# Kernel optimization log

Measured on AMD Instinct MI355X. Metric: run time of the kernel, lower is better.

Reference implementation:

```python
import jax, jax.numpy as jnp
import numpy as np

NJ, NS = 30000, 12000            # num job / skill nodes
E_JS, E_SJ, E_SS = 300000, 300000, 150000
SBERT, HID, OUT = 384, 128, 128
H = 2                             # GAT heads (concat=True)
NEG_SLOPE = 0.2


def setup_inputs() -> dict:
    key = jax.random.key(0)
    ks = iter(jax.random.split(key, 64))
    nrm = lambda shape, s=1.0: jax.random.normal(next(ks), shape, jnp.float32) * s
    ridx = lambda n, hi: jax.random.randint(next(ks), (n,), 0, hi, jnp.int32)
    W = 0.05  # weight scale to keep activations sane across layers
    return dict(
        x_job=nrm((NJ, SBERT)), x_skill=nrm((NS, SBERT)),
        ei_js_src=ridx(E_JS, NJ), ei_js_dst=ridx(E_JS, NS),
        ei_sj_src=ridx(E_SJ, NS), ei_sj_dst=ridx(E_SJ, NJ),
        ei_ss_src=ridx(E_SS, NS), ei_ss_dst=ridx(E_SS, NS),
        query=nrm((SBERT,)),
        W0_job=nrm((SBERT, HID), W), b0_job=jnp.zeros((HID,), jnp.float32),
        g0_job=jnp.ones((HID,), jnp.float32), be0_job=jnp.zeros((HID,), jnp.float32),
        W0_skill=nrm((SBERT, HID), W), b0_skill=jnp.zeros((HID,), jnp.float32),
        g0_skill=jnp.ones((HID,), jnp.float32), be0_skill=jnp.zeros((HID,), jnp.float32),
        gat_Ws=nrm((2, 3, HID, H * HID), W), gat_Wd=nrm((2, 3, HID, H * HID), W),
        gat_as=nrm((2, 3, H, HID), W), gat_ad=nrm((2, 3, H, HID), W),
        gat_b=jnp.zeros((2, 3, H * HID), jnp.float32),
        inter_W=nrm((2, 2, H * HID, HID), W), inter_b=jnp.zeros((2, 2, HID), jnp.float32),
        Wjf=nrm((HID, OUT), W), bjf=jnp.zeros((OUT,), jnp.float32),
        Wq=nrm((SBERT, OUT), W), bq=jnp.zeros((OUT,), jnp.float32),
    )


def _layer_norm(x, g, b):
    mu = x.mean(-1, keepdims=True)
    var = ((x - mu) ** 2).mean(-1, keepdims=True)
    return (x - mu) * jax.lax.rsqrt(var + 1e-5) * g + b


def _gat(x_src, x_dst, src, dst, Ws, Wd, a_s, a_d, bias, num_dst):
    # PyG GATConv: lin_src/lin_dst (no bias), additive attention, scatter-softmax over dst.
    hs = (x_src @ Ws).reshape(-1, H, HID)            # [Ns,H,C]
    hd = (x_dst @ Wd).reshape(-1, H, HID)            # [Nd,H,C]
    e = jax.nn.leaky_relu((hs * a_s).sum(-1)[src] + (hd * a_d).sum(-1)[dst], NEG_SLOPE)  # [E,H]
    m = jax.ops.segment_max(e, dst, num_segments=num_dst)
    p = jnp.exp(e - m[dst])
    den = jax.ops.segment_sum(p, dst, num_segments=num_dst)
    w = p / (den[dst] + 1e-16)                       # [E,H]
    out = jax.ops.segment_sum(hs[src] * w[:, :, None], dst, num_segments=num_dst)
    return out.reshape(num_dst, H * HID) + bias


def _forward(x_job, x_skill, query,
             W0_job, b0_job, g0_job, be0_job, W0_skill, b0_skill, g0_skill, be0_skill,
             gat_Ws, gat_Wd, gat_as, gat_ad, gat_b, inter_W, inter_b, Wjf, bjf, Wq, bq,
             ei_js_src, ei_js_dst, ei_sj_src, ei_sj_dst, ei_ss_src, ei_ss_dst):
    # initial per-type lin + LN + relu (dropout = identity in eval)
    xj = jax.nn.relu(_layer_norm(x_job @ W0_job + b0_job, g0_job, be0_job))
    xs = jax.nn.relu(_layer_norm(x_skill @ W0_skill + b0_skill, g0_skill, be0_skill))
    # skill->skill relation adds self loops (src == dst node type)
    loops = jnp.arange(NS, dtype=jnp.int32)
    ss_src = jnp.concatenate([ei_ss_src, loops])
    ss_dst = jnp.concatenate([ei_ss_dst, loops])
    for i in range(2):  # num_layers
        o_s = (_gat(xj, xs, ei_js_src, ei_js_dst, gat_Ws[i, 0], gat_Wd[i, 0],
                    gat_as[i, 0], gat_ad[i, 0], gat_b[i, 0], NS)
               + _gat(xs, xs, ss_src, ss_dst, gat_Ws[i, 2], gat_Wd[i, 2],
                      gat_as[i, 2], gat_ad[i, 2], gat_b[i, 2], NS))  # HeteroConv aggr='sum'
        o_j = _gat(xs, xj, ei_sj_src, ei_sj_dst, gat_Ws[i, 1], gat_Wd[i, 1],
                   gat_as[i, 1], gat_ad[i, 1], gat_b[i, 1], NJ)
        xj = jax.nn.relu(o_j @ inter_W[i, 0] + inter_b[i, 0])
        xs = jax.nn.relu(o_s @ inter_W[i, 1] + inter_b[i, 1])
    job_emb = xj @ Wjf + bjf                          # [NJ,OUT]
    q = query @ Wq + bq                               # [OUT]
    scores = job_emb @ q                              # [NJ]
    return scores, job_emb, q


def reference(x_job, x_skill, ei_js_src, ei_js_dst, ei_sj_src, ei_sj_dst,
              ei_ss_src, ei_ss_dst, query,
              W0_job, b0_job, g0_job, be0_job, W0_skill, b0_skill, g0_skill, be0_skill,
              gat_Ws, gat_Wd, gat_as, gat_ad, gat_b, inter_W, inter_b,
              Wjf, bjf, Wq, bq):
    return _forward(x_job, x_skill, query,
                    W0_job, b0_job, g0_job, be0_job, W0_skill, b0_skill, g0_skill, be0_skill,
                    gat_Ws, gat_Wd, gat_as, gat_ad, gat_b, inter_W, inter_b, Wjf, bjf, Wq, bq,
                    ei_js_src, ei_js_dst, ei_sj_src, ei_sj_dst, ei_ss_src, ei_ss_dst)
```

## Files before the change

kernel.cpp:

```cpp
#include <hip/hip_runtime.h>
#include <hip/hip_bf16.h>
#include <math.h>

#define NJ 30000
#define NS 12000
#define E_JS 300000
#define E_SJ 300000
#define E_SS 150000
#define ETOT (E_JS + E_SJ + E_SS + NS)
#define NBINS (NS + NJ + NS)
#define NBUK ((NBINS + 63) / 64)
#define SBERT 384
#define HIST_NB 512
#define SCAT_NB 480
#define CAST_MATS 14
#define CAST_BPM 48
#define PREP_CAST (CAST_MATS * CAST_BPM)
#define PREP_WA   (PREP_CAST + 192)
#define PREP_QV   PREP_WA
#define PREP_GB   (PREP_QV + 1)
#define PREP_HIST (PREP_GB + 1)

static inline int cdiv(int a, int b) { return (a + b - 1) / b; }

typedef __attribute__((ext_vector_type(8))) short bf8_t;
typedef __attribute__((ext_vector_type(4))) float f4_t;
typedef unsigned short u16;

__device__ inline float bf2f(unsigned short u) {
    union { unsigned int i; float f; } z; z.i = ((unsigned int)u) << 16; return z.f;
}
__device__ inline unsigned short f2bf(float f) {
    unsigned int x = __float_as_uint(f);
    unsigned int r = (x + 0x7fffu + ((x >> 16) & 1u)) >> 16;
    return (unsigned short)r;
}

__device__ inline void edge_decode(int e, const int* js_src, const int* js_dst,
                                   const int* sj_src, const int* sj_dst,
                                   const int* ss_src, const int* ss_dst,
                                   int& src, int& bin) {
    if (e < E_JS) { src = js_src[e]; bin = js_dst[e]; }
    else if (e < E_JS + E_SJ) { int i = e - E_JS; src = sj_src[i]; bin = NS + sj_dst[i]; }
    else if (e < E_JS + E_SJ + E_SS) { int i = e - E_JS - E_SJ; src = ss_src[i]; bin = NS + NJ + ss_dst[i]; }
    else { int i = e - E_JS - E_SJ - E_SS; src = i; bin = NS + NJ + i; }
}

struct CastT { const float* src; unsigned short* dst; int K; int N; int srcLd; int dstLd; };
struct PrepArgs {
    CastT m[CAST_MATS];
    const float* Ws; const float* as_; const float* Wd; const float* ad_;
    float* wsa; float* wda; int* bcnt;
    const float* query; const float* Wq; const float* bq; float* qv;
    const float* gat_b; float* gbS;
    const int* js_src; const int* js_dst;
    const int* sj_src; const int* sj_dst;
    const int* ss_src; const int* ss_dst;
};

__global__ __launch_bounds__(256) void k_prep(PrepArgs A) {
    __shared__ float ldt[32][33];
    __shared__ int lh[NBUK];
    int b = blockIdx.x;
    if (b < PREP_CAST) {
        int mi = b / CAST_BPM, bx = b % CAST_BPM;
        CastT cm = A.m[mi];
        int tilesN = cm.N >> 5;
        int total = (cm.K >> 5) * tilesN;
        if (bx >= total) return;
        int tk = bx / tilesN, tn = bx % tilesN;
        int k0 = tk * 32, n0 = tn * 32;
        int col = threadIdx.x & 31;
        int row0 = threadIdx.x >> 5;
#pragma unroll
        for (int r = 0; r < 4; ++r) {
            int kk = row0 + r * 8;
            ldt[kk][col] = cm.src[(size_t)(k0 + kk) * cm.srcLd + n0 + col];
        }
        __syncthreads();
#pragma unroll
        for (int r = 0; r < 4; ++r) {
            int nn = row0 + r * 8;
            cm.dst[(size_t)(n0 + nn) * cm.dstLd + k0 + col] = f2bf(ldt[col][nn]);
        }
    } else if (b < PREP_WA) {
        int qw = ((b - PREP_CAST) * 256 + threadIdx.x) >> 4;
        int cl = threadIdx.x & 15;
        if (qw < 2 * 1536) {
            int which = qw / 1536;
            int r = qw % 1536;
            int lr = r / 256;
            int kh = r % 256;
            int k = kh / 2, h = kh % 2;
            const float* W = which ? A.Wd : A.Ws;
            const float* a = which ? A.ad_ : A.as_;
            const float* wrow = W + ((size_t)(lr * 128 + k)) * 256 + h * 128 + cl * 8;
            const float* arow = a + (size_t)(lr * 2 + h) * 128 + cl * 8;
            float4 w0 = *(const float4*)wrow, w1 = *(const float4*)(wrow + 4);
            float4 a0 = *(const float4*)arow, a1 = *(const float4*)(arow + 4);
            float acc = w0.x * a0.x + w0.y * a0.y + w0.z * a0.z + w0.w * a0.w
                      + w1.x * a1.x + w1.y * a1.y + w1.z * a1.z + w1.w * a1.w;
            acc += __shfl_xor(acc, 1, 64);
            acc += __shfl_xor(acc, 2, 64);
            acc += __shfl_xor(acc, 4, 64);
            acc += __shfl_xor(acc, 8, 64);
            if (cl == 0) (which ? A.wda : A.wsa)[lr * 256 + k * 2 + h] = acc;
        }
    } else if (b == PREP_QV) {
        int c = threadIdx.x;
        if (c < 128) {
            float acc = A.bq[c];
            for (int k = 0; k < SBERT; ++k) acc += A.query[k] * A.Wq[(size_t)k * 128 + c];
            A.qv[c] = acc;
        }
    } else if (b == PREP_GB) {
        int c = threadIdx.x;
        if (c < 256) A.gbS[c] = A.gat_b[c] + A.gat_b[512 + c];
    } else {
        int t = threadIdx.x;
        for (int i = t; i < NBUK; i += 256) lh[i] = 0;
        __syncthreads();
        int hb = b - PREP_HIST;
        for (int e = hb * 256 + t; e < ETOT; e += HIST_NB * 256) {
            int src, bin;
            edge_decode(e, A.js_src, A.js_dst, A.sj_src, A.sj_dst, A.ss_src, A.ss_dst, src, bin);
            atomicAdd(&lh[bin >> 6], 1);
        }
        __syncthreads();
        for (int i = t; i < NBUK; i += 256) {
            int v = lh[i];
            if (v) atomicAdd(&A.bcnt[i], v);
        }
    }
}

struct GJob {
    const void* X; const unsigned short* Wt;
    const float* bias; const float* gamma; const float* beta;
    void* Y; int M; int K; int N; int ldY; int srcf32;
    const float* qv; float* sc;
    int aMode = 0;
    const float* wav0 = nullptr; const float* wav1 = nullptr;
    const float* wav2 = nullptr; const float* wav3 = nullptr;
    float* aOut = nullptr; int aStride = 0;
};
struct GPair { GJob a; GJob b; int blocksA; };

template <int EPI>
__device__ void mgemm_body(const GPair& P, int bx) {
    int mb = bx;
    GJob g = (mb < P.blocksA) ? P.a : P.b;
    if (mb >= P.blocksA) mb -= P.blocksA;
    const int row0 = mb * 64;

    __shared__ __align__(16) float As[4][64][32];
    __shared__ __align__(16) unsigned short Bs[4][128][32];
    const int t = threadIdx.x;
    const int wave = t >> 6, lane = t & 63;
    const int q = lane >> 4, c = lane & 15;
    const int K = g.K;
    const float* Xf = (const float*)g.X;

    f4_t acc[8];
#pragma unroll
    for (int nt = 0; nt < 8; ++nt) acc[nt] = (f4_t){0.f, 0.f, 0.f, 0.f};

    auto STAGE = [&](int cur, int k0) {
#pragma unroll
        for (int i = 0; i < 2; ++i) {
            int bi = i * 256 + t;
            int row = bi >> 3, b = bi & 7;
            int ra = row0 + row; ra = (ra < g.M) ? ra : (g.M - 1);
            const float* gsrc = Xf + (size_t)ra * K + k0 + ((b ^ (row & 7)) << 2);
            __builtin_amdgcn_global_load_lds(
                (__attribute__((address_space(1))) void*)gsrc,
                (__attribute__((address_space(3))) void*)((char*)&As[cur][0][0] + ((i * 4 + wave) << 10)),
                16, 0, 0);
        }
#pragma unroll
        for (int i = 0; i < 2; ++i) {
            int bi = i * 256 + t;
            int row = bi >> 2, b = bi & 3;
            const unsigned short* gsrc = g.Wt + (size_t)row * K + k0 + ((b ^ ((row >> 1) & 3)) << 3);
            __builtin_amdgcn_global_load_lds(
                (__attribute__((address_space(1))) void*)gsrc,
                (__attribute__((address_space(3))) void*)((char*)&Bs[cur][0][0] + ((i * 4 + wave) << 10)),
                16, 0, 0);
        }
    };

    auto MF = [&](int cur) {
        const char* Ab = (const char*)&As[cur][0][0];
        const char* Bb = (const char*)&Bs[cur][0][0];
        int r = wave * 16 + c;
        int sw = r & 7;
        f4_t fa0 = *(const f4_t*)(Ab + r * 128 + (((q * 2) ^ sw) << 4));
        f4_t fa1 = *(const f4_t*)(Ab + r * 128 + (((q * 2 + 1) ^ sw) << 4));
        bf8_t af;
        af[0] = (short)f2bf(fa0[0]); af[1] = (short)f2bf(fa0[1]);
        af[2] = (short)f2bf(fa0[2]); af[3] = (short)f2bf(fa0[3]);
        af[4] = (short)f2bf(fa1[0]); af[5] = (short)f2bf(fa1[1]);
        af[6] = (short)f2bf(fa1[2]); af[7] = (short)f2bf(fa1[3]);
#pragma unroll
        for (int nt = 0; nt < 8; ++nt) {
            int rb = nt * 16 + c;
            bf8_t bfr = *(const bf8_t*)(Bb + rb * 64 + ((q ^ ((rb >> 1) & 3)) << 4));
            acc[nt] = __builtin_amdgcn_mfma_f32_16x16x32_bf16(af, bfr, acc[nt], 0, 0, 0);
        }
    };

    STAGE(0, 0);
    STAGE(1, 32);
    STAGE(2, 64);
#pragma unroll
    for (int k = 0; k < 12; ++k) {
        if (k < 10)      asm volatile("s_waitcnt vmcnt(8)" ::: "memory");
        else if (k == 10) asm volatile("s_waitcnt vmcnt(4)" ::: "memory");
        else             asm volatile("s_waitcnt vmcnt(0)" ::: "memory");
        __builtin_amdgcn_s_barrier();
        asm volatile("" ::: "memory");
        if (k + 3 < 12) STAGE((k + 3) & 3, (k + 3) * 32);
        MF(k & 3);
    }

    float bcol[8], gcol[8], becol[8];
#pragma unroll
    for (int nt = 0; nt < 8; ++nt) {
        bcol[nt] = g.bias[nt * 16 + c];
        if constexpr (EPI == 3) {
            gcol[nt] = g.gamma[nt * 16 + c];
            becol[nt] = g.beta[nt * 16 + c];
        }
    }

#pragma unroll
    for (int r = 0; r < 4; ++r) {
        int grow = row0 + wave * 16 + q * 4 + r;
        float v[8];
#pragma unroll
        for (int nt = 0; nt < 8; ++nt) v[nt] = acc[nt][r] + bcol[nt];
        if constexpr (EPI == 3) {
            float s = 0.f, ss = 0.f;
#pragma unroll
            for (int nt = 0; nt < 8; ++nt) { s += v[nt]; ss += v[nt] * v[nt]; }
#pragma unroll
            for (int m = 8; m >= 1; m >>= 1) {
                s += __shfl_xor(s, m, 64);
                ss += __shfl_xor(ss, m, 64);
            }
            float mu = s * (1.f / 128.f);
            float var = ss * (1.f / 128.f) - mu * mu;
            float rs = rsqrtf(var + 1e-5f);
#pragma unroll
            for (int nt = 0; nt < 8; ++nt)
                v[nt] = fmaxf((v[nt] - mu) * rs * gcol[nt] + becol[nt], 0.f);
        }
        if (g.aMode > 0) {
            float pa[8];
#pragma unroll
            for (int i = 0; i < 8; ++i) pa[i] = 0.f;
#pragma unroll
            for (int nt = 0; nt < 8; ++nt) {
                int col = nt * 16 + c;
                float2 w0 = *(const float2*)&g.wav0[col * 2];
                pa[0] += v[nt] * w0.x; pa[1] += v[nt] * w0.y;
                if (g.aMode > 1) {
                    float2 w1 = *(const float2*)&g.wav1[col * 2];
                    pa[2] += v[nt] * w1.x; pa[3] += v[nt] * w1.y;
                }
                if (g.aMode > 2) {
                    float2 w2 = *(const float2*)&g.wav2[col * 2];
                    float2 w3 = *(const float2*)&g.wav3[col * 2];
                    pa[4] += v[nt] * w2.x; pa[5] += v[nt] * w2.y;
                    pa[6] += v[nt] * w3.x; pa[7] += v[nt] * w3.y;
                }
            }
#pragma unroll
            for (int m = 8; m >= 1; m >>= 1) {
                pa[0] += __shfl_xor(pa[0], m, 64); pa[1] += __shfl_xor(pa[1], m, 64);
                pa[2] += __shfl_xor(pa[2], m, 64); pa[3] += __shfl_xor(pa[3], m, 64);
                pa[4] += __shfl_xor(pa[4], m, 64); pa[5] += __shfl_xor(pa[5], m, 64);
                pa[6] += __shfl_xor(pa[6], m, 64); pa[7] += __shfl_xor(pa[7], m, 64);
            }
            if (c == 0 && grow < g.M) {
                float* ao = &g.aOut[(size_t)grow * g.aStride];
                ao[0] = pa[0]; ao[1] = pa[1];
                if (g.aMode > 1) { ao[2] = pa[2]; ao[3] = pa[3]; }
                if (g.aMode > 2) { ao[4] = pa[4]; ao[5] = pa[5]; ao[6] = pa[6]; ao[7] = pa[7]; }
            }
        }
        if (grow < g.M) {
            unsigned short* Y = (unsigned short*)g.Y;
#pragma unroll
            for (int nt = 0; nt < 8; ++nt)
                Y[(size_t)grow * g.ldY + nt * 16 + c] = f2bf(v[nt]);
        }
    }
}

__global__ __launch_bounds__(256) void k_scan(
    const int* __restrict__ bcnt, int* __restrict__ bukoff, int* __restrict__ bukcur) {
    __shared__ int sd[256];
    int t = threadIdx.x;
    int i0 = t * 4;
    int v0 = (i0 < NBUK) ? bcnt[i0] : 0;
    int v1 = (i0 + 1 < NBUK) ? bcnt[i0 + 1] : 0;
    int v2 = (i0 + 2 < NBUK) ? bcnt[i0 + 2] : 0;
    int v3 = (i0 + 3 < NBUK) ? bcnt[i0 + 3] : 0;
    int csum = v0 + v1 + v2 + v3;
    sd[t] = csum;
    __syncthreads();
    for (int off = 1; off < 256; off <<= 1) {
        int tmp = (t >= off) ? sd[t - off] : 0;
        __syncthreads();
        sd[t] += tmp;
        __syncthreads();
    }
    int excl = sd[t] - csum;
    int p0 = excl, p1 = excl + v0, p2 = excl + v0 + v1, p3 = excl + v0 + v1 + v2;
    if (i0 < NBUK) { bukoff[i0] = p0; bukcur[i0] = p0; }
    if (i0 + 1 < NBUK) { bukoff[i0 + 1] = p1; bukcur[i0 + 1] = p1; }
    if (i0 + 2 < NBUK) { bukoff[i0 + 2] = p2; bukcur[i0 + 2] = p2; }
    if (i0 + 3 < NBUK) { bukoff[i0 + 3] = p3; bukcur[i0 + 3] = p3; }
    if (t == 0) bukoff[NBUK] = ETOT;
}

__global__ __launch_bounds__(256) void k_lin0_scat(
    GPair P, int gemmBlocks,
    const int* __restrict__ js_src, const int* __restrict__ js_dst,
    const int* __restrict__ sj_src, const int* __restrict__ sj_dst,
    const int* __restrict__ ss_src, const int* __restrict__ ss_dst,
    int* __restrict__ bukcur, uint2* __restrict__ pairs) {
    if (blockIdx.x < (unsigned)gemmBlocks) {
        mgemm_body<3>(P, blockIdx.x);
        return;
    }
    __shared__ int lh[NBUK];
    __shared__ int lbase[NBUK];
    int t = threadIdx.x;
    int sb = blockIdx.x - gemmBlocks;
    const int CH = (ETOT + SCAT_NB - 1) / SCAT_NB;
    const int beg = sb * CH;
    const int endi = (beg + CH < ETOT) ? beg + CH : ETOT;
    if (beg >= ETOT) return;
    for (int i = t; i < NBUK; i += 256) lh[i] = 0;
    __syncthreads();
    for (int e = beg + t; e < endi; e += 256) {
        int src, bin;
        edge_decode(e, js_src, js_dst, sj_src, sj_dst, ss_src, ss_dst, src, bin);
        atomicAdd(&lh[bin >> 6], 1);
    }
    __syncthreads();
    for (int i = t; i < NBUK; i += 256) {
        int v = lh[i];
        lbase[i] = v ? atomicAdd(&bukcur[i], v) : 0;
    }
    __syncthreads();
    for (int i = t; i < NBUK; i += 256) lh[i] = 0;
    __syncthreads();
    for (int e = beg + t; e < endi; e += 256) {
        int src, bin;
        edge_decode(e, js_src, js_dst, sj_src, sj_dst, ss_src, ss_dst, src, bin);
        int bu = bin >> 6;
        int pos = lbase[bu] + atomicAdd(&lh[bu], 1);
        pairs[pos] = make_uint2((unsigned)src, (unsigned)bin);
    }
}

__global__ __launch_bounds__(256) void k_finalize(
    const uint2* __restrict__ pairs, const int* __restrict__ bukoff,
    int* __restrict__ offs, int* __restrict__ esrc) {
    int b = blockIdx.x, t = threadIdx.x;
    int base = bukoff[b], endi = bukoff[b + 1];
    __shared__ int cnt[64], excl[64], curs[64];
    if (t < 64) cnt[t] = 0;
    __syncthreads();
    for (int i = base + t; i < endi; i += 256)
        atomicAdd(&cnt[pairs[i].y & 63], 1);
    __syncthreads();
    if (t < 64) {
        int v = cnt[t];
        int inc = v;
#pragma unroll
        for (int off = 1; off < 64; off <<= 1) {
            int tmp = __shfl_up(inc, off, 64);
            if (t >= off) inc += tmp;
        }
        excl[t] = inc - v;
        curs[t] = inc - v;
    }
    __syncthreads();
    for (int i = base + t; i < endi; i += 256) {
        uint2 p = pairs[i];
        int lb = p.y & 63;
        int pos = atomicAdd(&curs[lb], 1);
        esrc[base + pos] = (int)p.x;
    }
    if (t < 64) {
        int bin = b * 64 + t;
        if (bin < NBINS) offs[bin] = base + excl[t];
    }
    if (b == 0 && t == 0) offs[NBINS] = ETOT;
}

__device__ inline void fm8(float p0, float p1, uint4 u, float a0[8], float a1[8]) {
    float x0 = __uint_as_float(u.x << 16);
    float x1 = __uint_as_float(u.x & 0xffff0000u);
    float x2 = __uint_as_float(u.y << 16);
    float x3 = __uint_as_float(u.y & 0xffff0000u);
    float x4 = __uint_as_float(u.z << 16);
    float x5 = __uint_as_float(u.z & 0xffff0000u);
    float x6 = __uint_as_float(u.w << 16);
    float x7 = __uint_as_float(u.w & 0xffff0000u);
    a0[0] += p0 * x0; a0[1] += p0 * x1; a0[2] += p0 * x2; a0[3] += p0 * x3;
    a0[4] += p0 * x4; a0[5] += p0 * x5; a0[6] += p0 * x6; a0[7] += p0 * x7;
    a1[0] += p1 * x0; a1[1] += p1 * x1; a1[2] += p1 * x2; a1[3] += p1 * x3;
    a1[4] += p1 * x4; a1[5] += p1 * x5; a1[6] += p1 * x6; a1[7] += p1 * x7;
}

__device__ inline void rel_run(
    const int* __restrict__ esrc, int beg, int end,
    const float* __restrict__ aSrc, int aShift, int aOff, float adx, float ady,
    const unsigned short* __restrict__ rows, int colOff, int g,
    float a0[8], float a1[8], float& den0, float& den1) {
    int j = beg;
    for (; j + 8 <= end; j += 8) {
        int s0 = esrc[j + g];
        int s1 = esrc[j + 4 + g];
        uint4 u0 = *(const uint4*)&rows[(unsigned)s0 * 128 + colOff];
        uint4 u1 = *(const uint4*)&rows[(unsigned)s1 * 128 + colOff];
        float2 f0 = *(const float2*)&aSrc[((unsigned)s0 << aShift) + aOff];
        float2 f1 = *(const float2*)&aSrc[((unsigned)s1 << aShift) + aOff];
        float e00 = f0.x + adx; e00 = e00 > 0.f ? e00 : 0.2f * e00;
        float e01 = f0.y + ady; e01 = e01 > 0.f ? e01 : 0.2f * e01;
        float e10 = f1.x + adx; e10 = e10 > 0.f ? e10 : 0.2f * e10;
        float e11 = f1.y + ady; e11 = e11 > 0.f ? e11 : 0.2f * e11;
        float p00 = __expf(e00), p01 = __expf(e01);
        float p10 = __expf(e10), p11 = __expf(e11);
        fm8(p00, p01, u0, a0, a1);
        fm8(p10, p11, u1, a0, a1);
        den0 += p00 + p10; den1 += p01 + p11;
    }
    for (; j < end; j += 4) {
        int e = j + g;
        bool ok = e < end;
        int s = esrc[ok ? e : j];
        uint4 u = *(const uint4*)&rows[(unsigned)s * 128 + colOff];
        float2 f = *(const float2*)&aSrc[((unsigned)s << aShift) + aOff];
        float e0 = f.x + adx; e0 = e0 > 0.f ? e0 : 0.2f * e0;
        float e1 = f.y + ady; e1 = e1 > 0.f ? e1 : 0.2f * e1;
        float p0 = ok ? __expf(e0) : 0.f;
        float p1 = ok ? __expf(e1) : 0.f;
        fm8(p0, p1, u, a0, a1);
        den0 += p0; den1 += p1;
    }
}

__device__ inline void store8(unsigned short* dst, const float v[8]) {
    uint4 o;
    o.x = (unsigned)f2bf(v[0]) | ((unsigned)f2bf(v[1]) << 16);
    o.y = (unsigned)f2bf(v[2]) | ((unsigned)f2bf(v[3]) << 16);
    o.z = (unsigned)f2bf(v[4]) | ((unsigned)f2bf(v[5]) << 16);
    o.w = (unsigned)f2bf(v[6]) | ((unsigned)f2bf(v[7]) << 16);
    *(uint4*)dst = o;
}

__device__ inline void finish_store(float a0[8], float a1[8], float den0, float den1,
                                    int lane, unsigned short* base) {
    float d0 = den0; d0 += __shfl_xor(d0, 16, 64); d0 += __shfl_xor(d0, 32, 64);
    float d1 = den1; d1 += __shfl_xor(d1, 16, 64); d1 += __shfl_xor(d1, 32, 64);
    float s0 = 1.f / (d0 + 1e-16f), s1 = 1.f / (d1 + 1e-16f);
    float o0[8], o1[8];
#pragma unroll
    for (int i = 0; i < 8; ++i) {
        float t0 = a0[i]; t0 += __shfl_xor(t0, 16, 64); t0 += __shfl_xor(t0, 32, 64);
        float t1 = a1[i]; t1 += __shfl_xor(t1, 16, 64); t1 += __shfl_xor(t1, 32, 64);
        o0[i] = t0 * s0; o1[i] = t1 * s1;
    }
    if ((lane >> 4) == 0) {
        store8(base, o0);
        store8(base + 128, o1);
    }
}

__global__ __launch_bounds__(256) void k_gather_all(
    const int* __restrict__ offs, const int* __restrict__ esrc,
    const float* __restrict__ aJ, const float* __restrict__ aS,
    const unsigned short* __restrict__ rowsJ,
    const unsigned short* __restrict__ rowsS,
    unsigned short* __restrict__ aggS,
    unsigned short* __restrict__ aggJ,
    int jobOnly) {
    int wave = threadIdx.x >> 6, lane = threadIdx.x & 63;
    int idx = blockIdx.x * 4 + wave;
    int g = lane >> 4, cl = lane & 15;
    int colOff = cl * 8;

    float a0[8], a1[8], den0, den1;

    if (jobOnly) {
        if (idx >= NJ) return;
        int d = idx;
#pragma unroll
        for (int i = 0; i < 8; ++i) { a0[i] = 0.f; a1[i] = 0.f; }
        den0 = den1 = 0.f;
        int bb = NS + d;
        float2 ad = *(const float2*)&aJ[(unsigned)d * 4 + 2];
        rel_run(esrc, offs[bb], offs[bb + 1], aS, 3, 4, ad.x, ad.y, rowsS, colOff, g, a0, a1, den0, den1);
        finish_store(a0, a1, den0, den1, lane, &aggJ[(size_t)d * 256 + colOff]);
        return;
    }
    if (idx < NS) {
        int d = idx;
#pragma unroll
        for (int i = 0; i < 8; ++i) { a0[i] = 0.f; a1[i] = 0.f; }
        den0 = den1 = 0.f;
        float2 adA = *(const float2*)&aS[(unsigned)d * 8 + 2];
        rel_run(esrc, offs[d], offs[d + 1], aJ, 2, 0, adA.x, adA.y, rowsJ, colOff, g, a0, a1, den0, den1);
        finish_store(a0, a1, den0, den1, lane, &aggS[(size_t)d * 512 + colOff]);
#pragma unroll
        for (int i = 0; i < 8; ++i) { a0[i] = 0.f; a1[i] = 0.f; }
        den0 = den1 = 0.f;
        int bb = NS + NJ + d;
        float2 adB = *(const float2*)&aS[(unsigned)d * 8 + 6];
        rel_run(esrc, offs[bb], offs[bb + 1], aS, 3, 0, adB.x, adB.y, rowsS, colOff, g, a0, a1, den0, den1);
        finish_store(a0, a1, den0, den1, lane, &aggS[(size_t)d * 512 + 256 + colOff]);
    } else if (idx < NS + NJ) {
        int d = idx - NS;
#pragma unroll
        for (int i = 0; i < 8; ++i) { a0[i] = 0.f; a1[i] = 0.f; }
        den0 = den1 = 0.f;
        int bb = NS + d;
        float2 ad = *(const float2*)&aJ[(unsigned)d * 4 + 2];
        rel_run(esrc, offs[bb], offs[bb + 1], aS, 3, 4, ad.x, ad.y, rowsS, colOff, g, a0, a1, den0, den1);
        finish_store(a0, a1, den0, den1, lane, &aggJ[(size_t)d * 256 + colOff]);
    }
}

struct FJob {
    const unsigned short* X; int K1; int M;
    const unsigned short* Wt1; const float* bias1;
    const unsigned short* Wt2; const float* bias2;
    const float* wa; float* aOut; int aStride;
    unsigned short* Y2;
};
struct FPair { FJob a; FJob b; int blocksA; };

__global__ __launch_bounds__(256) void k_fused2(FPair P) {
    int mb = blockIdx.x;
    FJob g = (mb < P.blocksA) ? P.a : P.b;
    if (mb >= P.blocksA) mb -= P.blocksA;
    const int row0 = mb * 64;
    const int K1 = g.K1;

    __shared__ __align__(16) unsigned short Al[64][40];
    __shared__ __align__(16) unsigned short Bl[128][40];
    __shared__ __align__(16) unsigned short Y1l[4][64][40];
    const int t = threadIdx.x;
    const int wave = t >> 6, lane = t & 63;
    const int q = lane >> 4, c = lane & 15;

    f4_t acc2[8];
#pragma unroll
    for (int nt = 0; nt < 8; ++nt) acc2[nt] = (f4_t){0.f, 0.f, 0.f, 0.f};

    for (int np = 0; np < 2; ++np) {
        f4_t acc[8];
#pragma unroll
        for (int nt = 0; nt < 8; ++nt) acc[nt] = (f4_t){0.f, 0.f, 0.f, 0.f};
        for (int k0 = 0; k0 < K1; k0 += 32) {
#pragma unroll
            for (int it = 0; it < 3; ++it) {
                int idx = t + it * 256;
                int r = idx >> 2, cc = (idx & 3) * 8;
                if (r < 64) {
                    int gr = row0 + r;
                    uint4 va = (gr < g.M) ? *(const uint4*)&g.X[(size_t)gr * K1 + k0 + cc]
                                          : make_uint4(0u, 0u, 0u, 0u);
                    *(uint4*)&Al[r][cc] = va;
                } else {
                    int br = r - 64;
                    *(uint4*)&Bl[br][cc] = *(const uint4*)&g.Wt1[(size_t)(np * 128 + br) * K1 + k0 + cc];
                }
            }
            __syncthreads();
            bf8_t af = *(const bf8_t*)&Al[wave * 16 + c][q * 8];
#pragma unroll
            for (int nt = 0; nt < 8; ++nt) {
                bf8_t bfr = *(const bf8_t*)&Bl[nt * 16 + c][q * 8];
                acc[nt] = __builtin_amdgcn_mfma_f32_16x16x32_bf16(af, bfr, acc[nt], 0, 0, 0);
            }
            __syncthreads();
        }
        float bcol[8];
#pragma unroll
        for (int nt = 0; nt < 8; ++nt) bcol[nt] = g.bias1[np * 128 + nt * 16 + c];
#pragma unroll
        for (int r = 0; r < 4; ++r) {
            int row = wave * 16 + q * 4 + r;
#pragma unroll
            for (int nt = 0; nt < 8; ++nt)
                Y1l[nt >> 1][row][(nt & 1) * 16 + c] = f2bf(acc[nt][r] + bcol[nt]);
        }
        __syncthreads();
        for (int k0 = 0; k0 < 128; k0 += 32) {
#pragma unroll
            for (int it = 0; it < 2; ++it) {
                int idx = t + it * 256;
                int br = idx >> 2, cc = (idx & 3) * 8;
                *(uint4*)&Bl[br][cc] = *(const uint4*)&g.Wt2[(size_t)br * 256 + np * 128 + k0 + cc];
            }
            __syncthreads();
            bf8_t af = *(const bf8_t*)&Y1l[k0 >> 5][wave * 16 + c][q * 8];
#pragma unroll
            for (int nt = 0; nt < 8; ++nt) {
                bf8_t bfr = *(const bf8_t*)&Bl[nt * 16 + c][q * 8];
                acc2[nt] = __builtin_amdgcn_mfma_f32_16x16x32_bf16(af, bfr, acc2[nt], 0, 0, 0);
            }
            __syncthreads();
        }
    }

    float b2[8];
#pragma unroll
    for (int nt = 0; nt < 8; ++nt) b2[nt] = g.bias2[nt * 16 + c];
#pragma unroll
    for (int r = 0; r < 4; ++r) {
        int grow = row0 + wave * 16 + q * 4 + r;
        float v[8];
#pragma unroll
        for (int nt = 0; nt < 8; ++nt) v[nt] = fmaxf(acc2[nt][r] + b2[nt], 0.f);
        if (g.wa) {
            float pa0 = 0.f, pa1 = 0.f;
#pragma unroll
            for (int nt = 0; nt < 8; ++nt) {
                float2 w0 = *(const float2*)&g.wa[(nt * 16 + c) * 2];
                pa0 += v[nt] * w0.x; pa1 += v[nt] * w0.y;
            }
#pragma unroll
            for (int m = 8; m >= 1; m >>= 1) {
                pa0 += __shfl_xor(pa0, m, 64);
                pa1 += __shfl_xor(pa1, m, 64);
            }
            if (c == 0 && grow < g.M) {
                g.aOut[(size_t)grow * g.aStride + 0] = pa0;
                g.aOut[(size_t)grow * g.aStride + 1] = pa1;
            }
        }
        if (g.Y2 && grow < g.M) {
#pragma unroll
            for (int nt = 0; nt < 8; ++nt)
                g.Y2[(size_t)grow * 128 + nt * 16 + c] = f2bf(v[nt]);
        }
    }
}

struct F3 {
    const unsigned short* X; int M;
    const unsigned short* Wt1; const float* bias1;
    const unsigned short* Wt2; const float* bias2;
    const unsigned short* Wt3; const float* bias3;
    const float* qv; float* sc; float* Y;
};

__global__ __launch_bounds__(256) void k_fused3(F3 g) {
    int mb = blockIdx.x;
    const int row0 = mb * 64;
    __shared__ __align__(16) unsigned short Al[64][40];
    __shared__ __align__(16) unsigned short Bl[128][40];
    __shared__ __align__(16) unsigned short Yl[4][64][40];
    const int t = threadIdx.x;
    const int wave = t >> 6, lane = t & 63;
    const int q = lane >> 4, c = lane & 15;

    f4_t acc2[8];
#pragma unroll
    for (int nt = 0; nt < 8; ++nt) acc2[nt] = (f4_t){0.f, 0.f, 0.f, 0.f};

    for (int np = 0; np < 2; ++np) {
        f4_t acc[8];
#pragma unroll
        for (int nt = 0; nt < 8; ++nt) acc[nt] = (f4_t){0.f, 0.f, 0.f, 0.f};
        for (int k0 = 0; k0 < 256; k0 += 32) {
#pragma unroll
            for (int it = 0; it < 3; ++it) {
                int idx = t + it * 256;
                int r = idx >> 2, cc = (idx & 3) * 8;
                if (r < 64) {
                    int gr = row0 + r;
                    uint4 va = (gr < g.M) ? *(const uint4*)&g.X[(size_t)gr * 256 + k0 + cc]
                                          : make_uint4(0u, 0u, 0u, 0u);
                    *(uint4*)&Al[r][cc] = va;
                } else {
                    int br = r - 64;
                    *(uint4*)&Bl[br][cc] = *(const uint4*)&g.Wt1[(size_t)(np * 128 + br) * 256 + k0 + cc];
                }
            }
            __syncthreads();
            bf8_t af = *(const bf8_t*)&Al[wave * 16 + c][q * 8];
#pragma unroll
            for (int nt = 0; nt < 8; ++nt) {
                bf8_t bfr = *(const bf8_t*)&Bl[nt * 16 + c][q * 8];
                acc[nt] = __builtin_amdgcn_mfma_f32_16x16x32_bf16(af, bfr, acc[nt], 0, 0, 0);
            }
            __syncthreads();
        }
        float bcol[8];
#pragma unroll
        for (int nt = 0; nt < 8; ++nt) bcol[nt] = g.bias1[np * 128 + nt * 16 + c];
#pragma unroll
        for (int r = 0; r < 4; ++r) {
            int row = wave * 16 + q * 4 + r;
#pragma unroll
            for (int nt = 0; nt < 8; ++nt)
                Yl[nt >> 1][row][(nt & 1) * 16 + c] = f2bf(acc[nt][r] + bcol[nt]);
        }
        __syncthreads();
        for (int k0 = 0; k0 < 128; k0 += 32) {
#pragma unroll
            for (int it = 0; it < 2; ++it) {
                int idx = t + it * 256;
                int br = idx >> 2, cc = (idx & 3) * 8;
                *(uint4*)&Bl[br][cc] = *(const uint4*)&g.Wt2[(size_t)br * 256 + np * 128 + k0 + cc];
            }
            __syncthreads();
            bf8_t af = *(const bf8_t*)&Yl[k0 >> 5][wave * 16 + c][q * 8];
#pragma unroll
            for (int nt = 0; nt < 8; ++nt) {
                bf8_t bfr = *(const bf8_t*)&Bl[nt * 16 + c][q * 8];
                acc2[nt] = __builtin_amdgcn_mfma_f32_16x16x32_bf16(af, bfr, acc2[nt], 0, 0, 0);
            }
            __syncthreads();
        }
    }

    {
        float b2[8];
#pragma unroll
        for (int nt = 0; nt < 8; ++nt) b2[nt] = g.bias2[nt * 16 + c];
#pragma unroll
        for (int r = 0; r < 4; ++r) {
            int row = wave * 16 + q * 4 + r;
#pragma unroll
            for (int nt = 0; nt < 8; ++nt)
                Yl[nt >> 1][row][(nt & 1) * 16 + c] = f2bf(fmaxf(acc2[nt][r] + b2[nt], 0.f));
        }
        __syncthreads();
    }

    f4_t acc3[8];
#pragma unroll
    for (int nt = 0; nt < 8; ++nt) acc3[nt] = (f4_t){0.f, 0.f, 0.f, 0.f};
    for (int k0 = 0; k0 < 128; k0 += 32) {
#pragma unroll
        for (int it = 0; it < 2; ++it) {
            int idx = t + it * 256;
            int br = idx >> 2, cc = (idx & 3) * 8;
            *(uint4*)&Bl[br][cc] = *(const uint4*)&g.Wt3[(size_t)br * 128 + k0 + cc];
        }
        __syncthreads();
        bf8_t af = *(const bf8_t*)&Yl[k0 >> 5][wave * 16 + c][q * 8];
#pragma unroll
        for (int nt = 0; nt < 8; ++nt) {
            bf8_t bfr = *(const bf8_t*)&Bl[nt * 16 + c][q * 8];
            acc3[nt] = __builtin_amdgcn_mfma_f32_16x16x32_bf16(af, bfr, acc3[nt], 0, 0, 0);
        }
        __syncthreads();
    }
    float b3[8], qcol[8];
#pragma unroll
    for (int nt = 0; nt < 8; ++nt) {
        b3[nt] = g.bias3[nt * 16 + c];
        qcol[nt] = g.qv[nt * 16 + c];
    }
#pragma unroll
    for (int r = 0; r < 4; ++r) {
        int grow = row0 + wave * 16 + q * 4 + r;
        float v[8];
#pragma unroll
        for (int nt = 0; nt < 8; ++nt) v[nt] = acc3[nt][r] + b3[nt];
        float part = 0.f;
#pragma unroll
        for (int nt = 0; nt < 8; ++nt) part += v[nt] * qcol[nt];
#pragma unroll
        for (int m = 8; m >= 1; m >>= 1) part += __shfl_xor(part, m, 64);
        if (grow < g.M) {
            if (c == 0) g.sc[grow] = part;
#pragma unroll
            for (int nt = 0; nt < 8; ++nt)
                g.Y[(size_t)grow * 128 + nt * 16 + c] = v[nt];
        }
    }
}

extern "C" void kernel_launch(void* const* d_in, const int* in_sizes, int n_in,
                              void* d_out, int out_size, void* d_ws, size_t ws_size,
                              hipStream_t stream) {
    const float* x_job   = (const float*)d_in[0];
    const float* x_skill = (const float*)d_in[1];
    const int* js_src = (const int*)d_in[2];
    const int* js_dst = (const int*)d_in[3];
    const int* sj_src = (const int*)d_in[4];
    const int* sj_dst = (const int*)d_in[5];
    const int* ss_src = (const int*)d_in[6];
    const int* ss_dst = (const int*)d_in[7];
    const float* query    = (const float*)d_in[8];
    const float* W0_job   = (const float*)d_in[9];
    const float* b0_job   = (const float*)d_in[10];
    const float* g0_job   = (const float*)d_in[11];
    const float* be0_job  = (const float*)d_in[12];
    const float* W0_skill = (const float*)d_in[13];
    const float* b0_skill = (const float*)d_in[14];
    const float* g0_skill = (const float*)d_in[15];
    const float* be0_skill= (const float*)d_in[16];
    const float* gat_Ws = (const float*)d_in[17];
    const float* gat_Wd = (const float*)d_in[18];
    const float* gat_as = (const float*)d_in[19];
    const float* gat_ad = (const float*)d_in[20];
    const float* gat_b  = (const float*)d_in[21];
    const float* inter_W = (const float*)d_in[22];
    const float* inter_b = (const float*)d_in[23];
    const float* Wjf = (const float*)d_in[24];
    const float* bjf = (const float*)d_in[25];
    const float* Wq  = (const float*)d_in[26];
    const float* bq  = (const float*)d_in[27];

    char* w = (char*)d_ws;
    auto alloc = [&](size_t bytes) -> void* {
        void* p = (void*)w;
        w += (bytes + 255) & ~(size_t)255;
        return p;
    };
    u16* xj   = (u16*)alloc((size_t)NJ * 128 * 2);
    u16* xs   = (u16*)alloc((size_t)NS * 128 * 2);
    u16* xs1  = (u16*)alloc((size_t)NS * 128 * 2);
    u16* aggJ  = (u16*)alloc((size_t)NJ * 256 * 2);
    u16* aggJ1 = (u16*)alloc((size_t)NJ * 256 * 2);
    u16* aggS  = (u16*)alloc((size_t)NS * 512 * 2);
    u16* WtW0j = (u16*)alloc((size_t)SBERT * 128 * 2);
    u16* WtW0s = (u16*)alloc((size_t)SBERT * 128 * 2);
    u16* WsS1  = (u16*)alloc((size_t)256 * 512 * 2);
    u16* WsJ0  = (u16*)alloc((size_t)256 * 256 * 2);
    u16* WsJ1  = (u16*)alloc((size_t)256 * 256 * 2);
    u16* WtI00 = (u16*)alloc((size_t)128 * 256 * 2);
    u16* WtI01 = (u16*)alloc((size_t)128 * 256 * 2);
    u16* WtI10 = (u16*)alloc((size_t)128 * 256 * 2);
    u16* WtJf  = (u16*)alloc((size_t)128 * 128 * 2);
    float* gbS = (float*)alloc(256 * 4);
    float* aJ = (float*)alloc((size_t)NJ * 4 * 4);
    float* aS = (float*)alloc((size_t)NS * 8 * 4);
    float* wsa = (float*)alloc(6 * 256 * 4);
    float* wda = (float*)alloc(6 * 256 * 4);
    int* bcnt   = (int*)alloc((size_t)NBUK * 4);
    int* bukoff = (int*)alloc((size_t)(NBUK + 1) * 4);
    int* bukcur = (int*)alloc((size_t)NBUK * 4);
    uint2* pairs = (uint2*)alloc((size_t)ETOT * 8);
    int* offs = (int*)alloc((size_t)(NBINS + 1) * 4);
    int* esrc = (int*)alloc((size_t)ETOT * 4);

    float* out = (float*)d_out;
    float* scores  = out;
    float* job_emb = out + NJ;
    float* qv      = out + NJ + (size_t)NJ * 128;

    const int mbJ = cdiv(NJ, 64);
    const int mbS = cdiv(NS, 64);
    const int gemmB = mbJ + mbS;

    hipMemsetAsync(bcnt, 0, (size_t)NBUK * 4, stream);
    hipMemsetAsync(WsS1, 0, (size_t)256 * 512 * 2, stream);
    hipMemsetAsync(WsJ0, 0, (size_t)256 * 256 * 2, stream);
    hipMemsetAsync(WsJ1, 0, (size_t)256 * 256 * 2, stream);

    {
        const size_t WS = (size_t)128 * 256;
        const size_t IW = (size_t)256 * 128;
        PrepArgs A;
        A.m[0]  = {W0_job,   WtW0j, SBERT, 128, 128, SBERT};
        A.m[1]  = {W0_skill, WtW0s, SBERT, 128, 128, SBERT};
        A.m[2]  = {gat_Ws + 0 * WS,       WsS1,                       128, 128, 256, 512};
        A.m[3]  = {gat_Ws + 0 * WS + 128, WsS1 + 128 * 512 + 128,     128, 128, 256, 512};
        A.m[4]  = {gat_Ws + 2 * WS,       WsS1 + 256,                 128, 128, 256, 512};
        A.m[5]  = {gat_Ws + 2 * WS + 128, WsS1 + 128 * 512 + 384,     128, 128, 256, 512};
        A.m[6]  = {gat_Ws + 1 * WS,       WsJ0,                       128, 128, 256, 256};
        A.m[7]  = {gat_Ws + 1 * WS + 128, WsJ0 + 128 * 256 + 128,     128, 128, 256, 256};
        A.m[8]  = {gat_Ws + 4 * WS,       WsJ1,                       128, 128, 256, 256};
        A.m[9]  = {gat_Ws + 4 * WS + 128, WsJ1 + 128 * 256 + 128,     128, 128, 256, 256};
        A.m[10] = {inter_W + 0 * IW, WtI00, 256, 128, 128, 256};
        A.m[11] = {inter_W + 1 * IW, WtI01, 256, 128, 128, 256};
        A.m[12] = {inter_W + 2 * IW, WtI10, 256, 128, 128, 256};
        A.m[13] = {Wjf, WtJf, 128, 128, 128, 128};
        A.Ws = gat_Ws; A.as_ = gat_as; A.Wd = gat_Wd; A.ad_ = gat_ad;
        A.wsa = wsa; A.wda = wda; A.bcnt = bcnt;
        A.query = query; A.Wq = Wq; A.bq = bq; A.qv = qv;
        A.gat_b = gat_b; A.gbS = gbS;
        A.js_src = js_src; A.js_dst = js_dst;
        A.sj_src = sj_src; A.sj_dst = sj_dst;
        A.ss_src = ss_src; A.ss_dst = ss_dst;
        k_prep<<<PREP_HIST + HIST_NB, 256, 0, stream>>>(A);
    }

    k_scan<<<1, 256, 0, stream>>>(bcnt, bukoff, bukcur);

    {
        GPair P;
        P.a = {x_job, WtW0j, b0_job, g0_job, be0_job, xj, NJ, SBERT, 128, 128, 1,
               nullptr, nullptr, 2, wsa + 0, wda + 256, nullptr, nullptr, aJ, 4};
        P.b = {x_skill, WtW0s, b0_skill, g0_skill, be0_skill, xs, NS, SBERT, 128, 128, 1,
               nullptr, nullptr, 4, wsa + 2 * 256, wda + 0, wsa + 1 * 256, wda + 2 * 256, aS, 8};
        P.blocksA = mbJ;
        k_lin0_scat<<<gemmB + SCAT_NB, 256, 0, stream>>>(
            P, gemmB, js_src, js_dst, sj_src, sj_dst, ss_src, ss_dst, bukcur, pairs);
    }

    k_finalize<<<NBUK, 256, 0, stream>>>(pairs, bukoff, offs, esrc);

    k_gather_all<<<cdiv(NS + NJ, 4), 256, 0, stream>>>(
        offs, esrc, aJ, aS, xj, xs, aggS, aggJ, 0);

    {
        FPair P;
        P.a = {aggJ, 256, NJ, WsJ0, gat_b + 256, WtI00, inter_b + 0,
               wda + 4 * 256, aJ + 2, 4, nullptr};
        P.b = {aggS, 512, NS, WsS1, gbS, WtI01, inter_b + 128,
               wsa + 4 * 256, aS + 4, 8, xs1};
        P.blocksA = mbJ;
        k_fused2<<<gemmB, 256, 0, stream>>>(P);
    }

    k_gather_all<<<cdiv(NJ, 4), 256, 0, stream>>>(
        offs, esrc, aJ, aS, nullptr, xs1, nullptr, aggJ1, 1);

    {
        F3 g3;
        g3.X = aggJ1; g3.M = NJ;
        g3.Wt1 = WsJ1; g3.bias1 = gat_b + 4 * 256;
        g3.Wt2 = WtI10; g3.bias2 = inter_b + 2 * 128;
        g3.Wt3 = WtJf; g3.bias3 = bjf;
        g3.qv = qv; g3.sc = scores; g3.Y = job_emb;
        k_fused3<<<mbJ, 256, 0, stream>>>(g3);
    }
}
```

Measured before the change: 340.2 us.

## Load GEMM operands directly from global memory instead of LDS pipeline

```diff
diff --git a/kernel.cpp b/kernel.cpp
--- a/kernel.cpp
+++ b/kernel.cpp
@@ -153,74 +153,34 @@
     if (mb >= P.blocksA) mb -= P.blocksA;
     const int row0 = mb * 64;
 
-    __shared__ __align__(16) float As[4][64][32];
-    __shared__ __align__(16) unsigned short Bs[4][128][32];
     const int t = threadIdx.x;
     const int wave = t >> 6, lane = t & 63;
     const int q = lane >> 4, c = lane & 15;
-    const int K = g.K;
     const float* Xf = (const float*)g.X;
 
     f4_t acc[8];
 #pragma unroll
     for (int nt = 0; nt < 8; ++nt) acc[nt] = (f4_t){0.f, 0.f, 0.f, 0.f};
 
-    auto STAGE = [&](int cur, int k0) {
-#pragma unroll
-        for (int i = 0; i < 2; ++i) {
-            int bi = i * 256 + t;
-            int row = bi >> 3, b = bi & 7;
-            int ra = row0 + row; ra = (ra < g.M) ? ra : (g.M - 1);
-            const float* gsrc = Xf + (size_t)ra * K + k0 + ((b ^ (row & 7)) << 2);
-            __builtin_amdgcn_global_load_lds(
-                (__attribute__((address_space(1))) void*)gsrc,
-                (__attribute__((address_space(3))) void*)((char*)&As[cur][0][0] + ((i * 4 + wave) << 10)),
-                16, 0, 0);
-        }
-#pragma unroll
-        for (int i = 0; i < 2; ++i) {
-            int bi = i * 256 + t;
-            int row = bi >> 2, b = bi & 3;
-            const unsigned short* gsrc = g.Wt + (size_t)row * K + k0 + ((b ^ ((row >> 1) & 3)) << 3);
-            __builtin_amdgcn_global_load_lds(
-                (__attribute__((address_space(1))) void*)gsrc,
-                (__attribute__((address_space(3))) void*)((char*)&Bs[cur][0][0] + ((i * 4 + wave) << 10)),
-                16, 0, 0);
-        }
-    };
-
-    auto MF = [&](int cur) {
-        const char* Ab = (const char*)&As[cur][0][0];
-        const char* Bb = (const char*)&Bs[cur][0][0];
-        int r = wave * 16 + c;
-        int sw = r & 7;
-        f4_t fa0 = *(const f4_t*)(Ab + r * 128 + (((q * 2) ^ sw) << 4));
-        f4_t fa1 = *(const f4_t*)(Ab + r * 128 + (((q * 2 + 1) ^ sw) << 4));
+    int rowA = row0 + wave * 16 + c;
+    rowA = (rowA < g.M) ? rowA : (g.M - 1);
+    const float* pa = Xf + (size_t)rowA * SBERT + q * 8;
+    const unsigned short* pb = g.Wt + (size_t)c * SBERT + q * 8;
+
+#pragma unroll
+    for (int k0 = 0; k0 < SBERT; k0 += 32) {
+        float4 fa0 = *(const float4*)(pa + k0);
+        float4 fa1 = *(const float4*)(pa + k0 + 4);
         bf8_t af;
-        af[0] = (short)f2bf(fa0[0]); af[1] = (short)f2bf(fa0[1]);
-        af[2] = (short)f2bf(fa0[2]); af[3] = (short)f2bf(fa0[3]);
-        af[4] = (short)f2bf(fa1[0]); af[5] = (short)f2bf(fa1[1]);
-        af[6] = (short)f2bf(fa1[2]); af[7] = (short)f2bf(fa1[3]);
+        af[0] = (short)f2bf(fa0.x); af[1] = (short)f2bf(fa0.y);
+        af[2] = (short)f2bf(fa0.z); af[3] = (short)f2bf(fa0.w);
+        af[4] = (short)f2bf(fa1.x); af[5] = (short)f2bf(fa1.y);
+        af[6] = (short)f2bf(fa1.z); af[7] = (short)f2bf(fa1.w);
 #pragma unroll
         for (int nt = 0; nt < 8; ++nt) {
-            int rb = nt * 16 + c;
-            bf8_t bfr = *(const bf8_t*)(Bb + rb * 64 + ((q ^ ((rb >> 1) & 3)) << 4));
+            bf8_t bfr = *(const bf8_t*)(pb + (size_t)nt * 16 * SBERT + k0);
             acc[nt] = __builtin_amdgcn_mfma_f32_16x16x32_bf16(af, bfr, acc[nt], 0, 0, 0);
         }
-    };
-
-    STAGE(0, 0);
-    STAGE(1, 32);
-    STAGE(2, 64);
-#pragma unroll
-    for (int k = 0; k < 12; ++k) {
-        if (k < 10)      asm volatile("s_waitcnt vmcnt(8)" ::: "memory");
-        else if (k == 10) asm volatile("s_waitcnt vmcnt(4)" ::: "memory");
-        else             asm volatile("s_waitcnt vmcnt(0)" ::: "memory");
-        __builtin_amdgcn_s_barrier();
-        asm volatile("" ::: "memory");
-        if (k + 3 < 12) STAGE((k + 3) & 3, (k + 3) * 32);
-        MF(k & 3);
     }
 
     float bcol[8], gcol[8], becol[8];
@@ -256,37 +216,37 @@
                 v[nt] = fmaxf((v[nt] - mu) * rs * gcol[nt] + becol[nt], 0.f);
         }
         if (g.aMode > 0) {
-            float pa[8];
-#pragma unroll
-            for (int i = 0; i < 8; ++i) pa[i] = 0.f;
+            float pa2[8];
+#pragma unroll
+            for (int i = 0; i < 8; ++i) pa2[i] = 0.f;
 #pragma unroll
             for (int nt = 0; nt < 8; ++nt) {
                 int col = nt * 16 + c;
                 float2 w0 = *(const float2*)&g.wav0[col * 2];
-                pa[0] += v[nt] * w0.x; pa[1] += v[nt] * w0.y;
+                pa2[0] += v[nt] * w0.x; pa2[1] += v[nt] * w0.y;
                 if (g.aMode > 1) {
                     float2 w1 = *(const float2*)&g.wav1[col * 2];
-                    pa[2] += v[nt] * w1.x; pa[3] += v[nt] * w1.y;
+                    pa2[2] += v[nt] * w1.x; pa2[3] += v[nt] * w1.y;
                 }
                 if (g.aMode > 2) {
                     float2 w2 = *(const float2*)&g.wav2[col * 2];
                     float2 w3 = *(const float2*)&g.wav3[col * 2];
-                    pa[4] += v[nt] * w2.x; pa[5] += v[nt] * w2.y;
-                    pa[6] += v[nt] * w3.x; pa[7] += v[nt] * w3.y;
+                    pa2[4] += v[nt] * w2.x; pa2[5] += v[nt] * w2.y;
+                    pa2[6] += v[nt] * w3.x; pa2[7] += v[nt] * w3.y;
                 }
             }
 #pragma unroll
             for (int m = 8; m >= 1; m >>= 1) {
-                pa[0] += __shfl_xor(pa[0], m, 64); pa[1] += __shfl_xor(pa[1], m, 64);
-                pa[2] += __shfl_xor(pa[2], m, 64); pa[3] += __shfl_xor(pa[3], m, 64);
-                pa[4] += __shfl_xor(pa[4], m, 64); pa[5] += __shfl_xor(pa[5], m, 64);
-                pa[6] += __shfl_xor(pa[6], m, 64); pa[7] += __shfl_xor(pa[7], m, 64);
+                pa2[0] += __shfl_xor(pa2[0], m, 64); pa2[1] += __shfl_xor(pa2[1], m, 64);
+                pa2[2] += __shfl_xor(pa2[2], m, 64); pa2[3] += __shfl_xor(pa2[3], m, 64);
+                pa2[4] += __shfl_xor(pa2[4], m, 64); pa2[5] += __shfl_xor(pa2[5], m, 64);
+                pa2[6] += __shfl_xor(pa2[6], m, 64); pa2[7] += __shfl_xor(pa2[7], m, 64);
             }
             if (c == 0 && grow < g.M) {
                 float* ao = &g.aOut[(size_t)grow * g.aStride];
-                ao[0] = pa[0]; ao[1] = pa[1];
-                if (g.aMode > 1) { ao[2] = pa[2]; ao[3] = pa[3]; }
-                if (g.aMode > 2) { ao[4] = pa[4]; ao[5] = pa[5]; ao[6] = pa[6]; ao[7] = pa[7]; }
+                ao[0] = pa2[0]; ao[1] = pa2[1];
+                if (g.aMode > 1) { ao[2] = pa2[2]; ao[3] = pa2[3]; }
+                if (g.aMode > 2) { ao[4] = pa2[4]; ao[5] = pa2[5]; ao[6] = pa2[6]; ao[7] = pa2[7]; }
             }
         }
         if (grow < g.M) {
```

After: 338.4 us. Within noise of the previous version (-0.5%).

## Compute both N-halves per A tile in fused kernels; double-buffer mgemm

Applied to the files above, without the earlier changes.

```diff
diff --git a/kernel.cpp b/kernel.cpp
--- a/kernel.cpp
+++ b/kernel.cpp
@@ -153,8 +153,8 @@
     if (mb >= P.blocksA) mb -= P.blocksA;
     const int row0 = mb * 64;
 
-    __shared__ __align__(16) float As[4][64][32];
-    __shared__ __align__(16) unsigned short Bs[4][128][32];
+    __shared__ __align__(16) float As[2][64][32];
+    __shared__ __align__(16) unsigned short Bs[2][128][32];
     const int t = threadIdx.x;
     const int wave = t >> 6, lane = t & 63;
     const int q = lane >> 4, c = lane & 15;
@@ -210,17 +210,13 @@
     };
 
     STAGE(0, 0);
-    STAGE(1, 32);
-    STAGE(2, 64);
-#pragma unroll
-    for (int k = 0; k < 12; ++k) {
-        if (k < 10)      asm volatile("s_waitcnt vmcnt(8)" ::: "memory");
-        else if (k == 10) asm volatile("s_waitcnt vmcnt(4)" ::: "memory");
-        else             asm volatile("s_waitcnt vmcnt(0)" ::: "memory");
-        __builtin_amdgcn_s_barrier();
-        asm volatile("" ::: "memory");
-        if (k + 3 < 12) STAGE((k + 3) & 3, (k + 3) * 32);
-        MF(k & 3);
+    int cur = 0;
+    for (int k0 = 0; k0 < K; k0 += 32) {
+        asm volatile("s_waitcnt vmcnt(0)" ::: "memory");
+        __syncthreads();
+        if (k0 + 32 < K) STAGE(cur ^ 1, k0 + 32);
+        MF(cur);
+        cur ^= 1;
     }
 
     float bcol[8], gcol[8], becol[8];
@@ -554,44 +550,49 @@
     const int K1 = g.K1;
 
     __shared__ __align__(16) unsigned short Al[64][40];
-    __shared__ __align__(16) unsigned short Bl[128][40];
+    __shared__ __align__(16) unsigned short Bl[256][40];
     __shared__ __align__(16) unsigned short Y1l[4][64][40];
     const int t = threadIdx.x;
     const int wave = t >> 6, lane = t & 63;
     const int q = lane >> 4, c = lane & 15;
 
-    f4_t acc2[8];
-#pragma unroll
-    for (int nt = 0; nt < 8; ++nt) acc2[nt] = (f4_t){0.f, 0.f, 0.f, 0.f};
-
+    f4_t acc0[8], acc1[8], acc2[8];
+#pragma unroll
+    for (int nt = 0; nt < 8; ++nt) {
+        acc0[nt] = (f4_t){0.f, 0.f, 0.f, 0.f};
+        acc1[nt] = (f4_t){0.f, 0.f, 0.f, 0.f};
+        acc2[nt] = (f4_t){0.f, 0.f, 0.f, 0.f};
+    }
+
+    for (int k0 = 0; k0 < K1; k0 += 32) {
+#pragma unroll
+        for (int it = 0; it < 5; ++it) {
+            int idx = t + it * 256;
+            int r = idx >> 2, cc = (idx & 3) * 8;
+            if (r < 64) {
+                int gr = row0 + r;
+                uint4 va = (gr < g.M) ? *(const uint4*)&g.X[(size_t)gr * K1 + k0 + cc]
+                                      : make_uint4(0u, 0u, 0u, 0u);
+                *(uint4*)&Al[r][cc] = va;
+            } else {
+                int br = r - 64;
+                *(uint4*)&Bl[br][cc] = *(const uint4*)&g.Wt1[(size_t)br * K1 + k0 + cc];
+            }
+        }
+        __syncthreads();
+        bf8_t af = *(const bf8_t*)&Al[wave * 16 + c][q * 8];
+#pragma unroll
+        for (int nt = 0; nt < 8; ++nt) {
+            bf8_t b0 = *(const bf8_t*)&Bl[nt * 16 + c][q * 8];
+            acc0[nt] = __builtin_amdgcn_mfma_f32_16x16x32_bf16(af, b0, acc0[nt], 0, 0, 0);
+            bf8_t b1 = *(const bf8_t*)&Bl[128 + nt * 16 + c][q * 8];
+            acc1[nt] = __builtin_amdgcn_mfma_f32_16x16x32_bf16(af, b1, acc1[nt], 0, 0, 0);
+        }
+        __syncthreads();
+    }
+
+#pragma unroll
     for (int np = 0; np < 2; ++np) {
-        f4_t acc[8];
-#pragma unroll
-        for (int nt = 0; nt < 8; ++nt) acc[nt] = (f4_t){0.f, 0.f, 0.f, 0.f};
-        for (int k0 = 0; k0 < K1; k0 += 32) {
-#pragma unroll
-            for (int it = 0; it < 3; ++it) {
-                int idx = t + it * 256;
-                int r = idx >> 2, cc = (idx & 3) * 8;
-                if (r < 64) {
-                    int gr = row0 + r;
-                    uint4 va = (gr < g.M) ? *(const uint4*)&g.X[(size_t)gr * K1 + k0 + cc]
-                                          : make_uint4(0u, 0u, 0u, 0u);
-                    *(uint4*)&Al[r][cc] = va;
-                } else {
-                    int br = r - 64;
-                    *(uint4*)&Bl[br][cc] = *(const uint4*)&g.Wt1[(size_t)(np * 128 + br) * K1 + k0 + cc];
-                }
-            }
-            __syncthreads();
-            bf8_t af = *(const bf8_t*)&Al[wave * 16 + c][q * 8];
-#pragma unroll
-            for (int nt = 0; nt < 8; ++nt) {
-                bf8_t bfr = *(const bf8_t*)&Bl[nt * 16 + c][q * 8];
-                acc[nt] = __builtin_amdgcn_mfma_f32_16x16x32_bf16(af, bfr, acc[nt], 0, 0, 0);
-            }
-            __syncthreads();
-        }
         float bcol[8];
 #pragma unroll
         for (int nt = 0; nt < 8; ++nt) bcol[nt] = g.bias1[np * 128 + nt * 16 + c];
@@ -599,8 +600,10 @@
         for (int r = 0; r < 4; ++r) {
             int row = wave * 16 + q * 4 + r;
 #pragma unroll
-            for (int nt = 0; nt < 8; ++nt)
-                Y1l[nt >> 1][row][(nt & 1) * 16 + c] = f2bf(acc[nt][r] + bcol[nt]);
+            for (int nt = 0; nt < 8; ++nt) {
+                float vv = (np ? acc1[nt][r] : acc0[nt][r]) + bcol[nt];
+                Y1l[nt >> 1][row][(nt & 1) * 16 + c] = f2bf(vv);
+            }
         }
         __syncthreads();
         for (int k0 = 0; k0 < 128; k0 += 32) {
@@ -667,44 +670,49 @@
     int mb = blockIdx.x;
     const int row0 = mb * 64;
     __shared__ __align__(16) unsigned short Al[64][40];
-    __shared__ __align__(16) unsigned short Bl[128][40];
+    __shared__ __align__(16) unsigned short Bl[256][40];
     __shared__ __align__(16) unsigned short Yl[4][64][40];
     const int t = threadIdx.x;
     const int wave = t >> 6, lane = t & 63;
     const int q = lane >> 4, c = lane & 15;
 
-    f4_t acc2[8];
-#pragma unroll
-    for (int nt = 0; nt < 8; ++nt) acc2[nt] = (f4_t){0.f, 0.f, 0.f, 0.f};
-
+    f4_t acc0[8], acc1[8], acc2[8];
+#pragma unroll
+    for (int nt = 0; nt < 8; ++nt) {
+        acc0[nt] = (f4_t){0.f, 0.f, 0.f, 0.f};
+        acc1[nt] = (f4_t){0.f, 0.f, 0.f, 0.f};
+        acc2[nt] = (f4_t){0.f, 0.f, 0.f, 0.f};
+    }
+
+    for (int k0 = 0; k0 < 256; k0 += 32) {
+#pragma unroll
+        for (int it = 0; it < 5; ++it) {
+            int idx = t + it * 256;
+            int r = idx >> 2, cc = (idx & 3) * 8;
+            if (r < 64) {
+                int gr = row0 + r;
+                uint4 va = (gr < g.M) ? *(const uint4*)&g.X[(size_t)gr * 256 + k0 + cc]
+                                      : make_uint4(0u, 0u, 0u, 0u);
+                *(uint4*)&Al[r][cc] = va;
+            } else {
+                int br = r - 64;
+                *(uint4*)&Bl[br][cc] = *(const uint4*)&g.Wt1[(size_t)br * 256 + k0 + cc];
+            }
+        }
+        __syncthreads();
+        bf8_t af = *(const bf8_t*)&Al[wave * 16 + c][q * 8];
+#pragma unroll
+        for (int nt = 0; nt < 8; ++nt) {
+            bf8_t b0 = *(const bf8_t*)&Bl[nt * 16 + c][q * 8];
+            acc0[nt] = __builtin_amdgcn_mfma_f32_16x16x32_bf16(af, b0, acc0[nt], 0, 0, 0);
+            bf8_t b1 = *(const bf8_t*)&Bl[128 + nt * 16 + c][q * 8];
+            acc1[nt] = __builtin_amdgcn_mfma_f32_16x16x32_bf16(af, b1, acc1[nt], 0, 0, 0);
+        }
+        __syncthreads();
+    }
+
+#pragma unroll
     for (int np = 0; np < 2; ++np) {
-        f4_t acc[8];
-#pragma unroll
-        for (int nt = 0; nt < 8; ++nt) acc[nt] = (f4_t){0.f, 0.f, 0.f, 0.f};
-        for (int k0 = 0; k0 < 256; k0 += 32) {
-#pragma unroll
-            for (int it = 0; it < 3; ++it) {
-                int idx = t + it * 256;
-                int r = idx >> 2, cc = (idx & 3) * 8;
-                if (r < 64) {
-                    int gr = row0 + r;
-                    uint4 va = (gr < g.M) ? *(const uint4*)&g.X[(size_t)gr * 256 + k0 + cc]
-                                          : make_uint4(0u, 0u, 0u, 0u);
-                    *(uint4*)&Al[r][cc] = va;
-                } else {
-                    int br = r - 64;
-                    *(uint4*)&Bl[br][cc] = *(const uint4*)&g.Wt1[(size_t)(np * 128 + br) * 256 + k0 + cc];
-                }
-            }
-            __syncthreads();
-            bf8_t af = *(const bf8_t*)&Al[wave * 16 + c][q * 8];
-#pragma unroll
-            for (int nt = 0; nt < 8; ++nt) {
-                bf8_t bfr = *(const bf8_t*)&Bl[nt * 16 + c][q * 8];
-                acc[nt] = __builtin_amdgcn_mfma_f32_16x16x32_bf16(af, bfr, acc[nt], 0, 0, 0);
-            }
-            __syncthreads();
-        }
         float bcol[8];
 #pragma unroll
         for (int nt = 0; nt < 8; ++nt) bcol[nt] = g.bias1[np * 128 + nt * 16 + c];
@@ -712,8 +720,10 @@
         for (int r = 0; r < 4; ++r) {
             int row = wave * 16 + q * 4 + r;
 #pragma unroll
-            for (int nt = 0; nt < 8; ++nt)
-                Yl[nt >> 1][row][(nt & 1) * 16 + c] = f2bf(acc[nt][r] + bcol[nt]);
+            for (int nt = 0; nt < 8; ++nt) {
+                float vv = (np ? acc1[nt][r] : acc0[nt][r]) + bcol[nt];
+                Yl[nt >> 1][row][(nt & 1) * 16 + c] = f2bf(vv);
+            }
         }
         __syncthreads();
         for (int k0 = 0; k0 < 128; k0 += 32) {
```

Result: faster. 332.1 us (-2.4%).
